# Kernel optimization log

Measured on AMD Instinct MI355X. Metric: run time of the kernel, lower is better.

The kernel has to match this reference:

```python
import jax, jax.numpy as jnp
import numpy as np

B = 65536
H = 50          # hidden_size
L = 6           # num_layers
IN = 3          # input_size
T = 3           # seq_len


def setup_inputs() -> dict:
    key = jax.random.key(0)
    ks = jax.random.split(key, 10)
    s = 0.1  # weight init scale
    return {
        "x":     jax.random.normal(ks[0], (B, IN, T), dtype=jnp.float32),
        "h0":    jax.random.normal(ks[1], (L, B, H), dtype=jnp.float32),
        "c0":    jax.random.normal(ks[2], (L, B, H), dtype=jnp.float32),
        "w_ih0": jax.random.normal(ks[3], (4 * H, IN), dtype=jnp.float32) * s,
        "w_ih":  jax.random.normal(ks[4], (L - 1, 4 * H, H), dtype=jnp.float32) * s,
        "w_hh":  jax.random.normal(ks[5], (L, 4 * H, H), dtype=jnp.float32) * s,
        "b_ih":  jax.random.normal(ks[6], (L, 4 * H), dtype=jnp.float32) * s,
        "b_hh":  jax.random.normal(ks[7], (L, 4 * H), dtype=jnp.float32) * s,
        "fc_w":  jax.random.normal(ks[8], (1, H), dtype=jnp.float32) * s,
        "fc_b":  jax.random.normal(ks[9], (1,), dtype=jnp.float32) * s,
    }


def _lstm_layer(x_seq, h, c, w_ih, w_hh, b):
    """x_seq: [T, B, in]; returns all hidden states [T, B, H].
    PyTorch gate order: i, f, g, o."""
    def step(carry, x_t):
        h, c = carry
        gates = x_t @ w_ih.T + h @ w_hh.T + b  # [B, 4H]
        i, f, g, o = jnp.split(gates, 4, axis=-1)
        i = jax.nn.sigmoid(i)
        f = jax.nn.sigmoid(f)
        g = jnp.tanh(g)
        o = jax.nn.sigmoid(o)
        c = f * c + i * g
        h = o * jnp.tanh(c)
        return (h, c), h

    _, ys = jax.lax.scan(step, (h, c), x_seq)
    return ys


def reference(x, h0, c0, w_ih0, w_ih, w_hh, b_ih, b_hh, fc_w, fc_b):
    # original forward: input.permute(0, 2, 1) -> [B, T, IN], batch_first LSTM
    seq = jnp.transpose(x, (2, 0, 1))  # [T, B, IN] (time-major for scan)
    b = b_ih + b_hh                    # combined bias per layer [L, 4H]
    ys = _lstm_layer(seq, h0[0], c0[0], w_ih0, w_hh[0], b[0])
    for l in range(1, L):
        ys = _lstm_layer(ys, h0[l], c0[l], w_ih[l - 1], w_hh[l], b[l])
    # dropout(0.2) is identity in eval mode; take last timestep then fc
    last = ys[-1]                      # [B, H]
    return last @ fc_w.T + fc_b        # [B, 1]
```

## Files before the change

### kernel.cpp

```cpp
#include <hip/hip_runtime.h>


namespace {

constexpr int H  = 50;
constexpr int L  = 6;
constexpr int T  = 3;
constexpr int IN = 3;
constexpr int M  = 64;
constexpr int BLK = 512;
constexpr int ROWS = 72;

using half8 = __attribute__((ext_vector_type(8))) _Float16;
using f32x4 = __attribute__((ext_vector_type(4))) float;

__device__ __forceinline__ float fexp(float x) { return __builtin_amdgcn_exp2f(x * 1.44269504088896f); }
__device__ __forceinline__ float sigm(float x) { return __builtin_amdgcn_rcpf(1.f + fexp(-x)); }
__device__ __forceinline__ float tanh_(float x) { return 1.f - 2.f * __builtin_amdgcn_rcpf(1.f + fexp(2.f * x)); }

__global__ void wprep(const float* __restrict__ w_ih0, const float* __restrict__ w_ihL,
                      const float* __restrict__ w_hh,  const float* __restrict__ b_ih,
                      const float* __restrict__ b_hh,  _Float16* __restrict__ wbuf) {
  int t = blockIdx.x * 256 + threadIdx.x;
  if (t >= 384 * 64) return;
  int lam = t & 63, f = t >> 6;
  int nt = f & 15, s = (f >> 4) & 3, l = f >> 6;
  int n = nt * 16 + (lam & 15);
  int j = n >> 2, gate = n & 3, row = gate * 50 + j;
  _Float16 o8[8];
#pragma unroll
  for (int jj = 0; jj < 8; ++jj) {
    int k = s * 32 + (lam >> 4) * 8 + jj;
    float v = 0.f;
    if (j < H) {
      if (s < 2) {
        int ksz = (l == 0) ? IN : H;
        if (k < ksz) v = (l == 0) ? w_ih0[row * IN + k]
                                  : w_ihL[((size_t)(l - 1) * 200 + row) * H + k];
      } else {
        int kh = k - 64;
        if (kh < H)        v = w_hh[((size_t)l * 200 + row) * H + kh];
        else if (kh == 63) v = b_ih[l * 200 + row] + b_hh[l * 200 + row];
      }
    }
    o8[jj] = (_Float16)v;
  }
  ((half8*)wbuf)[t] = *(half8*)o8;
}

__global__ __launch_bounds__(BLK, 4)
void lstm_mfma(const float* __restrict__ x,   const float* __restrict__ h0,
               const float* __restrict__ c0,  const float* __restrict__ fc_w,
               const float* __restrict__ fc_b, const _Float16* __restrict__ wbuf,
               float* __restrict__ out, int B) {
  const int tid = threadIdx.x;
  const int lam = tid & 63;
  const int q   = lam >> 4;
  const int lm  = lam & 15;
  const int bbase = blockIdx.x * M;
  const int ng  = __builtin_amdgcn_readfirstlane(tid >> 6);
  const int ntp = __builtin_amdgcn_readfirstlane((ng + blockIdx.x) & 7);
  const int ntg0 = 2 * ntp, ntg1 = 2 * ntp + 1;
  const bool live0 = (ntg0 <= 12);
  const bool live1 = (ntg1 <= 12);

  __shared__ __align__(16) _Float16 ys[2][T][M][ROWS];

  for (int idx = tid; idx < T * M * 64; idx += BLK) {
    int t = idx >> 12, m = (idx >> 6) & 63, k = idx & 63;
    float v = (k < IN) ? x[(size_t)(bbase + m) * (IN * T) + k * T + t]
                       : (k == 63 ? 1.f : 0.f);
    ys[0][t][m][k] = (_Float16)v;
    ys[1][t][m][k] = (_Float16)((k == 63) ? 1.f : 0.f);
  }

  float c[2][4];
  f32x4 acc[2][4];
  half8 W[2][4];

  for (int l = 0; l < L; ++l) {
    const int sb = l & 1, db = sb ^ 1;
#pragma unroll
    for (int nt = 0; nt < 2; ++nt) {
      const int ntg = nt ? ntg1 : ntg0;
      const bool lv = nt ? live1 : live0;
      const int j = 4 * ntg + q;
#pragma unroll
      for (int mt = 0; mt < 4; ++mt)
        c[nt][mt] = (lv && j < H)
            ? c0[((size_t)l * B + bbase + mt * 16 + lm) * H + j] : 0.f;
    }
#pragma unroll
    for (int nt = 0; nt < 2; ++nt) {
      const int ntg = nt ? ntg1 : ntg0;
      const bool lv = nt ? live1 : live0;
      if (lv)
#pragma unroll
        for (int s = 0; s < 4; ++s)
          W[nt][s] = ((const half8*)wbuf)[((l * 4 + s) * 16 + ntg) * 64 + lam];
    }
    for (int idx = tid; idx < M * 64; idx += BLK) {
      int m = idx >> 6, k = idx & 63;
      float v = (k < H) ? h0[((size_t)l * B + bbase + m) * H + k]
                        : (k == 63 ? 1.f : 0.f);
      ys[db][T - 1][m][k] = (_Float16)v;
    }
    __syncthreads();

#pragma unroll
    for (int t = 0; t < T; ++t) {
      const int hs = (t == 0) ? T - 1 : t - 1;
#pragma unroll
      for (int nt = 0; nt < 2; ++nt)
#pragma unroll
        for (int mt = 0; mt < 4; ++mt) acc[nt][mt] = (f32x4){0.f, 0.f, 0.f, 0.f};

      if (live0) {
#pragma unroll
        for (int s = 0; s < 4; ++s) {
          const _Float16* base = (s < 2) ? &ys[sb][t][0][0] : &ys[db][hs][0][0];
          const int koff = (s & 1) * 32;
          half8 Xf[4];
#pragma unroll
          for (int mt = 0; mt < 4; ++mt)
            Xf[mt] = *(const half8*)(base + (mt * 16 + lm) * ROWS + koff + q * 8);
#pragma unroll
          for (int mt = 0; mt < 4; ++mt)
            acc[0][mt] = __builtin_amdgcn_mfma_f32_16x16x32_f16(W[0][s], Xf[mt], acc[0][mt], 0, 0, 0);
          if (live1)
#pragma unroll
            for (int mt = 0; mt < 4; ++mt)
              acc[1][mt] = __builtin_amdgcn_mfma_f32_16x16x32_f16(W[1][s], Xf[mt], acc[1][mt], 0, 0, 0);
        }

#pragma unroll
        for (int nt = 0; nt < 2; ++nt) {
          const int ntg = nt ? ntg1 : ntg0;
          const bool lv = nt ? live1 : live0;
          if (!lv) continue;
          const int j = 4 * ntg + q;
#pragma unroll
          for (int mt = 0; mt < 4; ++mt) {
            float ig = sigm(acc[nt][mt][0]);
            float fg = sigm(acc[nt][mt][1]);
            float gg = tanh_(acc[nt][mt][2]);
            float og = sigm(acc[nt][mt][3]);
            float cv = fg * c[nt][mt] + ig * gg;
            c[nt][mt] = cv;
            float hv = og * tanh_(cv);
            if (j < H)
              ys[db][t][mt * 16 + lm][j] = (_Float16)hv;
          }
        }
      }
      __syncthreads();
    }
  }

  {
    int m = tid >> 3, strip = tid & 7;
    float part = 0.f;
#pragma unroll
    for (int jj = 0; jj < 7; ++jj) {
      int j = strip + 8 * jj;
      if (j < H) part += fc_w[j] * (float)ys[0][T - 1][m][j];
    }
    part += __shfl_xor(part, 4);
    part += __shfl_xor(part, 2);
    part += __shfl_xor(part, 1);
    if (strip == 0) out[bbase + m] = part + fc_b[0];
  }
}

}

extern "C" void kernel_launch(void* const* d_in, const int* in_sizes, int n_in,
                              void* d_out, int out_size, void* d_ws, size_t ws_size,
                              hipStream_t stream) {
  const float* x     = (const float*)d_in[0];
  const float* h0    = (const float*)d_in[1];
  const float* c0    = (const float*)d_in[2];
  const float* w_ih0 = (const float*)d_in[3];
  const float* w_ih  = (const float*)d_in[4];
  const float* w_hh  = (const float*)d_in[5];
  const float* b_ih  = (const float*)d_in[6];
  const float* b_hh  = (const float*)d_in[7];
  const float* fc_w  = (const float*)d_in[8];
  const float* fc_b  = (const float*)d_in[9];
  float* out         = (float*)d_out;

  const int B = in_sizes[0] / (IN * T);
  _Float16* wbuf = (_Float16*)d_ws;

  wprep<<<(384 * 64 + 255) / 256, 256, 0, stream>>>(w_ih0, w_ih, w_hh, b_ih, b_hh, wbuf);
  lstm_mfma<<<B / M, BLK, 0, stream>>>(x, h0, c0, fc_w, fc_b, wbuf, out, B);
}
```

Measured before the change: 314.3 us.

## Precompute input projection before barrier, fold log2e scaling into weights, vectorize init

The input-projection MFMAs (x_t·W_ih) for the next timestep are now issued before the barrier, right after the gate update. Only the recurrent h·W_hh part stays on the critical path after each sync. Layer 0 skips the second input K-slice because it is all zero. Weights and biases are prescaled by log2(e) (doubled for the g gate), so each activation needs only exp2 and rcp. Shared-memory init is vectorized with explicit padding and bias-one columns, h0 loads use float2, and the cost is higher register pressure from keeping xa live across the barrier.

```diff
diff --git a/kernel.cpp b/kernel.cpp
--- a/kernel.cpp
+++ b/kernel.cpp
@@ -11,12 +11,12 @@
 constexpr int BLK = 512;
 constexpr int ROWS = 72;
 
-using half8 = __attribute__((ext_vector_type(8))) _Float16;
-using f32x4 = __attribute__((ext_vector_type(4))) float;
-
-__device__ __forceinline__ float fexp(float x) { return __builtin_amdgcn_exp2f(x * 1.44269504088896f); }
-__device__ __forceinline__ float sigm(float x) { return __builtin_amdgcn_rcpf(1.f + fexp(-x)); }
-__device__ __forceinline__ float tanh_(float x) { return 1.f - 2.f * __builtin_amdgcn_rcpf(1.f + fexp(2.f * x)); }
+using half8  = __attribute__((ext_vector_type(8))) _Float16;
+using half2v = __attribute__((ext_vector_type(2))) _Float16;
+using f32x4  = __attribute__((ext_vector_type(4))) float;
+
+__device__ __forceinline__ float rcp_(float x) { return __builtin_amdgcn_rcpf(x); }
+__device__ __forceinline__ float ex2(float x)  { return __builtin_amdgcn_exp2f(x); }
 
 __global__ void wprep(const float* __restrict__ w_ih0, const float* __restrict__ w_ihL,
                       const float* __restrict__ w_hh,  const float* __restrict__ b_ih,
@@ -27,6 +27,7 @@
   int nt = f & 15, s = (f >> 4) & 3, l = f >> 6;
   int n = nt * 16 + (lam & 15);
   int j = n >> 2, gate = n & 3, row = gate * 50 + j;
+  float scale = (gate == 2) ? 2.8853900817779268f : 1.4426950408889634f;
   _Float16 o8[8];
 #pragma unroll
   for (int jj = 0; jj < 8; ++jj) {
@@ -43,7 +44,7 @@
         else if (kh == 63) v = b_ih[l * 200 + row] + b_hh[l * 200 + row];
       }
     }
-    o8[jj] = (_Float16)v;
+    o8[jj] = (_Float16)(v * scale);
   }
   ((half8*)wbuf)[t] = *(half8*)o8;
 }
@@ -66,20 +67,38 @@
 
   __shared__ __align__(16) _Float16 ys[2][T][M][ROWS];
 
-  for (int idx = tid; idx < T * M * 64; idx += BLK) {
-    int t = idx >> 12, m = (idx >> 6) & 63, k = idx & 63;
-    float v = (k < IN) ? x[(size_t)(bbase + m) * (IN * T) + k * T + t]
-                       : (k == 63 ? 1.f : 0.f);
-    ys[0][t][m][k] = (_Float16)v;
-    ys[1][t][m][k] = (_Float16)((k == 63) ? 1.f : 0.f);
-  }
-
-  float c[2][4];
-  f32x4 acc[2][4];
+  if (tid < T * M) {
+    const int t = tid >> 6, m = tid & 63;
+    const float* xs = x + (size_t)(bbase + m) * (IN * T) + t;
+    _Float16* row = &ys[0][t][m][0];
+    half2v p0; p0[0] = (_Float16)xs[0]; p0[1] = (_Float16)xs[3];
+    half2v p1; p1[0] = (_Float16)xs[6]; p1[1] = (_Float16)0.f;
+    *(half2v*)(row)     = p0;
+    *(half2v*)(row + 2) = p1;
+#pragma unroll
+    for (int z = 0; z < 7; ++z)
+      *(unsigned long long*)(row + 4 + 4 * z) = 0ull;
+  }
+  if (tid < 2 * T * M) {
+    _Float16* row = &ys[0][0][0][0] + (size_t)tid * ROWS;
+#pragma unroll
+    for (int z = 0; z < 6; ++z)
+      *(unsigned int*)(row + 50 + 2 * z) = 0u;
+    half2v pb; pb[0] = (_Float16)0.f; pb[1] = (_Float16)1.f;
+    *(half2v*)(row + 62) = pb;
+  }
+  __syncthreads();
+
+  float cc[2][4];
+  f32x4 xa[2][4];
   half8 W[2][4];
+  const f32x4 z4 = {0.f, 0.f, 0.f, 0.f};
 
   for (int l = 0; l < L; ++l) {
     const int sb = l & 1, db = sb ^ 1;
+    _Float16 (*src)[M][ROWS] = ys[sb];
+    _Float16 (*dst)[M][ROWS] = ys[db];
+
 #pragma unroll
     for (int nt = 0; nt < 2; ++nt) {
       const int ntg = nt ? ntg1 : ntg0;
@@ -87,7 +106,7 @@
       const int j = 4 * ntg + q;
 #pragma unroll
       for (int mt = 0; mt < 4; ++mt)
-        c[nt][mt] = (lv && j < H)
+        cc[nt][mt] = (lv && j < H)
             ? c0[((size_t)l * B + bbase + mt * 16 + lm) * H + j] : 0.f;
     }
 #pragma unroll
@@ -99,57 +118,100 @@
         for (int s = 0; s < 4; ++s)
           W[nt][s] = ((const half8*)wbuf)[((l * 4 + s) * 16 + ntg) * 64 + lam];
     }
-    for (int idx = tid; idx < M * 64; idx += BLK) {
-      int m = idx >> 6, k = idx & 63;
-      float v = (k < H) ? h0[((size_t)l * B + bbase + m) * H + k]
-                        : (k == 63 ? 1.f : 0.f);
-      ys[db][T - 1][m][k] = (_Float16)v;
+
+    if (live0) {
+#pragma unroll
+      for (int s = 0; s < 2; ++s) {
+        if (s == 1 && l == 0) continue;
+        half8 Xf[4];
+#pragma unroll
+        for (int mt = 0; mt < 4; ++mt)
+          Xf[mt] = *(const half8*)(&src[0][mt * 16 + lm][s * 32 + q * 8]);
+#pragma unroll
+        for (int mt = 0; mt < 4; ++mt)
+          xa[0][mt] = __builtin_amdgcn_mfma_f32_16x16x32_f16(
+              W[0][s], Xf[mt], s == 0 ? z4 : xa[0][mt], 0, 0, 0);
+        if (live1)
+#pragma unroll
+          for (int mt = 0; mt < 4; ++mt)
+            xa[1][mt] = __builtin_amdgcn_mfma_f32_16x16x32_f16(
+                W[1][s], Xf[mt], s == 0 ? z4 : xa[1][mt], 0, 0, 0);
+      }
+    }
+
+    {
+      const int mg = tid >> 3, kpl = tid & 7;
+      const float* hp = h0 + ((size_t)l * B + bbase + mg) * H + 2 * kpl;
+      _Float16* dp = &dst[T - 1][mg][2 * kpl];
+#pragma unroll
+      for (int it = 0; it < 4; ++it) {
+        if (it < 3 || kpl == 0) {
+          float2 v = *(const float2*)(hp + 16 * it);
+          half2v pv; pv[0] = (_Float16)v.x; pv[1] = (_Float16)v.y;
+          *(half2v*)(dp + 16 * it) = pv;
+        }
+      }
     }
     __syncthreads();
 
 #pragma unroll
     for (int t = 0; t < T; ++t) {
-      const int hs = (t == 0) ? T - 1 : t - 1;
-#pragma unroll
-      for (int nt = 0; nt < 2; ++nt)
-#pragma unroll
-        for (int mt = 0; mt < 4; ++mt) acc[nt][mt] = (f32x4){0.f, 0.f, 0.f, 0.f};
-
+      const int hsl = (t == 0) ? T - 1 : t - 1;
       if (live0) {
 #pragma unroll
-        for (int s = 0; s < 4; ++s) {
-          const _Float16* base = (s < 2) ? &ys[sb][t][0][0] : &ys[db][hs][0][0];
-          const int koff = (s & 1) * 32;
+        for (int s = 0; s < 2; ++s) {
           half8 Xf[4];
 #pragma unroll
           for (int mt = 0; mt < 4; ++mt)
-            Xf[mt] = *(const half8*)(base + (mt * 16 + lm) * ROWS + koff + q * 8);
+            Xf[mt] = *(const half8*)(&dst[hsl][mt * 16 + lm][s * 32 + q * 8]);
 #pragma unroll
           for (int mt = 0; mt < 4; ++mt)
-            acc[0][mt] = __builtin_amdgcn_mfma_f32_16x16x32_f16(W[0][s], Xf[mt], acc[0][mt], 0, 0, 0);
+            xa[0][mt] = __builtin_amdgcn_mfma_f32_16x16x32_f16(
+                W[0][s + 2], Xf[mt], xa[0][mt], 0, 0, 0);
           if (live1)
 #pragma unroll
             for (int mt = 0; mt < 4; ++mt)
-              acc[1][mt] = __builtin_amdgcn_mfma_f32_16x16x32_f16(W[1][s], Xf[mt], acc[1][mt], 0, 0, 0);
+              xa[1][mt] = __builtin_amdgcn_mfma_f32_16x16x32_f16(
+                  W[1][s + 2], Xf[mt], xa[1][mt], 0, 0, 0);
         }
 
 #pragma unroll
         for (int nt = 0; nt < 2; ++nt) {
+          if (nt && !live1) continue;
           const int ntg = nt ? ntg1 : ntg0;
-          const bool lv = nt ? live1 : live0;
-          if (!lv) continue;
           const int j = 4 * ntg + q;
 #pragma unroll
           for (int mt = 0; mt < 4; ++mt) {
-            float ig = sigm(acc[nt][mt][0]);
-            float fg = sigm(acc[nt][mt][1]);
-            float gg = tanh_(acc[nt][mt][2]);
-            float og = sigm(acc[nt][mt][3]);
-            float cv = fg * c[nt][mt] + ig * gg;
-            c[nt][mt] = cv;
-            float hv = og * tanh_(cv);
+            const float ig = rcp_(1.f + ex2(-xa[nt][mt][0]));
+            const float fg = rcp_(1.f + ex2(-xa[nt][mt][1]));
+            const float gg = 2.f * rcp_(1.f + ex2(-xa[nt][mt][2])) - 1.f;
+            const float og = rcp_(1.f + ex2(-xa[nt][mt][3]));
+            const float cv = fg * cc[nt][mt] + ig * gg;
+            cc[nt][mt] = cv;
+            const float tc = 2.f * rcp_(1.f + ex2(-2.8853900817779268f * cv)) - 1.f;
+            const float hv = og * tc;
             if (j < H)
-              ys[db][t][mt * 16 + lm][j] = (_Float16)hv;
+              dst[t][mt * 16 + lm][j] = (_Float16)hv;
+          }
+        }
+
+        if (t < T - 1) {
+#pragma unroll
+          for (int s = 0; s < 2; ++s) {
+            if (s == 1 && l == 0) continue;
+            half8 Xf[4];
+#pragma unroll
+            for (int mt = 0; mt < 4; ++mt)
+              Xf[mt] = *(const half8*)(&src[t + 1][mt * 16 + lm][s * 32 + q * 8]);
+#pragma unroll
+            for (int mt = 0; mt < 4; ++mt)
+              xa[0][mt] = __builtin_amdgcn_mfma_f32_16x16x32_f16(
+                  W[0][s], Xf[mt], s == 0 ? z4 : xa[0][mt], 0, 0, 0);
+            if (live1)
+#pragma unroll
+              for (int mt = 0; mt < 4; ++mt)
+                xa[1][mt] = __builtin_amdgcn_mfma_f32_16x16x32_f16(
+                    W[1][s], Xf[mt], s == 0 ? z4 : xa[1][mt], 0, 0, 0);
           }
         }
       }
```

Measured after the change: 269.6 us. -14.2%, faster.
